# Optimization experiments

Hardware: AMD Instinct MI355X
Metric: run time of the kernel (lower is better)

## Reference

```python
import jax, jax.numpy as jnp
import numpy as np

KSIZE = 35
SIGMA = 0.3 * ((KSIZE - 1) * 0.5 - 1) + 0.8  # sigma_space == sigma_density == 5.6


def _gaussian_weight(k, sigma):
    # normalized 2D isotropic Gaussian, matching GaussianFilter.gaussian_weight
    g = jnp.arange(k, dtype=jnp.float32) - (k // 2)
    w = jnp.exp(-(g[:, None] ** 2 + g[None, :] ** 2) / (2.0 * sigma ** 2))
    return w / w.sum()


def setup_inputs() -> dict:
    key = jax.random.key(0)
    x = jax.random.uniform(key, (1, 3, 128, 128), dtype=jnp.float32)
    return {"x": x}


def reference(x):
    k = KSIZE
    pad = (k - 1) // 2
    B, C, H, W = x.shape
    xp = jnp.pad(x, ((0, 0), (0, 0), (pad, pad), (pad, pad)), mode='reflect')
    # unfold dims 2 and 3 -> patches [B, C, H, W, k, k]
    ri = jnp.arange(H)[:, None] + jnp.arange(k)[None, :]   # [H, k]
    rj = jnp.arange(W)[:, None] + jnp.arange(k)[None, :]   # [W, k]
    p = xp[:, :, ri, :]            # [B, C, H, k, W+2p]
    p = p[:, :, :, :, rj]          # [B, C, H, k, W, k]
    patches = jnp.transpose(p, (0, 1, 2, 4, 3, 5))  # [B, C, H, W, k, k]
    # density weights: channel-mean abs diff to center pixel
    dd = jnp.mean(jnp.abs(patches - x[..., None, None]), axis=1, keepdims=True)  # [B,1,H,W,k,k]
    wd = jnp.exp(-(dd ** 2) / (2.0 * SIGMA ** 2))
    wd = wd / wd.sum(axis=(-1, -2), keepdims=True)
    w = wd * _gaussian_weight(k, SIGMA)                    # [B,1,H,W,k,k]
    w_sum = w.sum(axis=(-1, -2))                           # [B,1,H,W]
    out = (w * patches).sum(axis=(-1, -2)) / w_sum         # [B,C,H,W]
    return out
```

## Files before the change

### kernel.cpp

```cpp
#include <hip/hip_runtime.h>
#include <math.h>

#define KS   35
#define PAD  17
#define H    128
#define W    128
#define NC   3
#define TILE 8
#define LW   (TILE + KS - 1)
#define BLK  256

__device__ __forceinline__ int reflect_idx(int p) {
    if (p < 0) p = -p;
    if (p >= H) p = 2 * H - 2 - p;
    return p;
}

__global__ __launch_bounds__(BLK)
void bilateral_kernel(const float* __restrict__ x, float* __restrict__ out) {
    __shared__ float s_in[NC][LW][LW];
    __shared__ float s_g[KS * KS];

    const int tid = threadIdx.x;
    const int tx0 = blockIdx.x * TILE;
    const int ty0 = blockIdx.y * TILE;

    const float sigma  = 5.6f;
    const float inv2s2 = 1.0f / (2.0f * sigma * sigma);

    for (int k = tid; k < KS * KS; k += BLK) {
        int di = k / KS, dj = k - di * KS;
        float r2 = (float)((di - PAD) * (di - PAD) + (dj - PAD) * (dj - PAD));
        s_g[k] = __expf(-r2 * inv2s2);
    }
    for (int idx = tid; idx < NC * LW * LW; idx += BLK) {
        int c   = idx / (LW * LW);
        int rem = idx - c * (LW * LW);
        int ly  = rem / LW, lx = rem - ly * LW;
        int gy  = reflect_idx(ty0 - PAD + ly);
        int gx  = reflect_idx(tx0 - PAD + lx);
        (&s_in[0][0][0])[idx] = x[(c * H + gy) * W + gx];
    }
    __syncthreads();

    const int sub = tid & 3;
    const int pix = tid >> 2;
    const int py  = pix >> 3, px = pix & 7;

    const float c0 = s_in[0][py + PAD][px + PAD];
    const float c1 = s_in[1][py + PAD][px + PAD];
    const float c2 = s_in[2][py + PAD][px + PAD];

    float n0 = 0.f, n1 = 0.f, n2 = 0.f, den = 0.f;
    for (int di = sub; di < KS; di += 4) {
        const float* r0 = &s_in[0][py + di][px];
        const float* r1 = &s_in[1][py + di][px];
        const float* r2 = &s_in[2][py + di][px];
        const float* gw = &s_g[di * KS];
        #pragma unroll 5
        for (int dj = 0; dj < KS; ++dj) {
            float p0 = r0[dj], p1 = r1[dj], p2 = r2[dj];
            float dd = (fabsf(p0 - c0) + fabsf(p1 - c1) + fabsf(p2 - c2)) * (1.0f / 3.0f);
            float wd = __expf(-dd * dd * inv2s2);
            float w  = wd * gw[dj];
            n0 = fmaf(w, p0, n0);
            n1 = fmaf(w, p1, n1);
            n2 = fmaf(w, p2, n2);
            den += w;
        }
    }

    for (int m = 1; m <= 2; m <<= 1) {
        n0  += __shfl_xor(n0, m);
        n1  += __shfl_xor(n1, m);
        n2  += __shfl_xor(n2, m);
        den += __shfl_xor(den, m);
    }

    if (sub == 0) {
        int gy = ty0 + py, gx = tx0 + px;
        float inv = 1.0f / den;
        out[(0 * H + gy) * W + gx] = n0 * inv;
        out[(1 * H + gy) * W + gx] = n1 * inv;
        out[(2 * H + gy) * W + gx] = n2 * inv;
    }
}

extern "C" void kernel_launch(void* const* d_in, const int* in_sizes, int n_in,
                              void* d_out, int out_size, void* d_ws, size_t ws_size,
                              hipStream_t stream) {
    const float* x = (const float*)d_in[0];
    float* out = (float*)d_out;
    dim3 grid(W / TILE, H / TILE);
    dim3 block(BLK);
    bilateral_kernel<<<grid, block, 0, stream>>>(x, out);
}
```

Baseline: 69.00 us.

## Fold spatial Gaussian into exp2 argument, interleave channels, shrink tile

Stores the three channels interleaved as 16-byte float4 entries in shared memory so each tap is one vector LDS load. The spatial Gaussian table is removed: its exponent is computed incrementally by finite differences and combined with the range term into a single exp2. The tile shrinks to 4x4 pixels with 16 threads per pixel, launching 4x more blocks with an occupancy hint. The cost is more reflect/global loads per output pixel (a larger relative halo) and a wider shuffle reduction.

```diff
diff --git a/kernel.cpp b/kernel.cpp
--- a/kernel.cpp
+++ b/kernel.cpp
@@ -5,10 +5,11 @@
 #define PAD  17
 #define H    128
 #define W    128
-#define NC   3
-#define TILE 8
+#define TILE 4
 #define LW   (TILE + KS - 1)
 #define BLK  256
+
+struct alignas(16) F4 { float c0, c1, c2, pd; };
 
 __device__ __forceinline__ int reflect_idx(int p) {
     if (p < 0) p = -p;
@@ -16,61 +17,63 @@
     return p;
 }
 
-__global__ __launch_bounds__(BLK)
+__global__ __launch_bounds__(BLK, 4)
 void bilateral_kernel(const float* __restrict__ x, float* __restrict__ out) {
-    __shared__ float s_in[NC][LW][LW];
-    __shared__ float s_g[KS * KS];
+    __shared__ F4 s_in[LW * LW];
 
     const int tid = threadIdx.x;
     const int tx0 = blockIdx.x * TILE;
     const int ty0 = blockIdx.y * TILE;
 
-    const float sigma  = 5.6f;
-    const float inv2s2 = 1.0f / (2.0f * sigma * sigma);
+    const float LOG2E = 1.4426950408889634f;
+    const float c_sp  = LOG2E / 62.72f;
+    const float c_rng = LOG2E / (62.72f * 9.0f);
 
-    for (int k = tid; k < KS * KS; k += BLK) {
-        int di = k / KS, dj = k - di * KS;
-        float r2 = (float)((di - PAD) * (di - PAD) + (dj - PAD) * (dj - PAD));
-        s_g[k] = __expf(-r2 * inv2s2);
-    }
-    for (int idx = tid; idx < NC * LW * LW; idx += BLK) {
-        int c   = idx / (LW * LW);
-        int rem = idx - c * (LW * LW);
-        int ly  = rem / LW, lx = rem - ly * LW;
-        int gy  = reflect_idx(ty0 - PAD + ly);
-        int gx  = reflect_idx(tx0 - PAD + lx);
-        (&s_in[0][0][0])[idx] = x[(c * H + gy) * W + gx];
+    for (int idx = tid; idx < LW * LW; idx += BLK) {
+        int ly = idx / LW, lx = idx - ly * LW;
+        int gy = reflect_idx(ty0 - PAD + ly);
+        int gx = reflect_idx(tx0 - PAD + lx);
+        F4 v;
+        v.c0 = x[gy * W + gx];
+        v.c1 = x[H * W + gy * W + gx];
+        v.c2 = x[2 * H * W + gy * W + gx];
+        v.pd = 0.0f;
+        s_in[idx] = v;
     }
     __syncthreads();
 
-    const int sub = tid & 3;
-    const int pix = tid >> 2;
-    const int py  = pix >> 3, px = pix & 7;
+    const int sub = tid & 15;
+    const int pix = tid >> 4;
+    const int px  = pix & 3, py = pix >> 2;
+    const int si  = sub & 3, sj = sub >> 2;
 
-    const float c0 = s_in[0][py + PAD][px + PAD];
-    const float c1 = s_in[1][py + PAD][px + PAD];
-    const float c2 = s_in[2][py + PAD][px + PAD];
+    const F4 c = s_in[(py + PAD) * LW + (px + PAD)];
+
+    float a   = -c_sp * (float)((si - PAD) * (si - PAD));
+    float ad  = -c_sp * (float)(8 * (si - PAD) + 16);
+    const float b0   = -c_sp * (float)((sj - PAD) * (sj - PAD));
+    const float bd0  = -c_sp * (float)(8 * (sj - PAD) + 16);
+    const float add2 = -32.0f * c_sp;
 
     float n0 = 0.f, n1 = 0.f, n2 = 0.f, den = 0.f;
-    for (int di = sub; di < KS; di += 4) {
-        const float* r0 = &s_in[0][py + di][px];
-        const float* r1 = &s_in[1][py + di][px];
-        const float* r2 = &s_in[2][py + di][px];
-        const float* gw = &s_g[di * KS];
-        #pragma unroll 5
-        for (int dj = 0; dj < KS; ++dj) {
-            float p0 = r0[dj], p1 = r1[dj], p2 = r2[dj];
-            float dd = (fabsf(p0 - c0) + fabsf(p1 - c1) + fabsf(p2 - c2)) * (1.0f / 3.0f);
-            float wd = __expf(-dd * dd * inv2s2);
-            float w  = wd * gw[dj];
-            n0 = fmaf(w, p0, n0);
-            n1 = fmaf(w, p1, n1);
-            n2 = fmaf(w, p2, n2);
+    for (int di = si; di < KS; di += 4) {
+        const F4* row = &s_in[(py + di) * LW + px];
+        float g  = a + b0;
+        float gd = bd0;
+        for (int dj = sj; dj < KS; dj += 4) {
+            F4 p = row[dj];
+            float s = fabsf(p.c0 - c.c0) + fabsf(p.c1 - c.c1) + fabsf(p.c2 - c.c2);
+            float w = __builtin_amdgcn_exp2f(fmaf(s * s, -c_rng, g));
+            n0 = fmaf(w, p.c0, n0);
+            n1 = fmaf(w, p.c1, n1);
+            n2 = fmaf(w, p.c2, n2);
             den += w;
+            g += gd; gd += add2;
         }
+        a += ad; ad += add2;
     }
 
-    for (int m = 1; m <= 2; m <<= 1) {
+    for (int m = 1; m <= 8; m <<= 1) {
         n0  += __shfl_xor(n0, m);
         n1  += __shfl_xor(n1, m);
         n2  += __shfl_xor(n2, m);
```

Measured after the change: 64.68 us. 6.3% less time.
